# Kernel optimization log

Hardware: AMD Instinct MI355X
Metric: run time of the kernel (lower is better)

Reference implementation:

```python
import jax, jax.numpy as jnp
import numpy as np

BEV_H = 100
BEV_W = 100
BEV_Z = 4
NUM_CAMS = 6
EMBED = 256
HF, WF = 32, 88
PC_RANGE = (-51.2, -51.2, -5.0, 51.2, 51.2, 3.0)
EPS = 1e-5


def setup_inputs() -> dict:
    key = jax.random.key(0)
    ks = jax.random.split(key, 5)
    B, Nq = 1, BEV_H * BEV_W
    return {
        "query": jax.random.normal(ks[0], (B, Nq, EMBED), jnp.float32),
        "img_feats": jax.random.normal(ks[1], (B, NUM_CAMS, EMBED, HF, WF), jnp.float32),
        "lidar2img": jax.random.normal(ks[2], (B, NUM_CAMS, 4, 4), jnp.float32),
        "attn_w": jax.random.normal(ks[3], (EMBED, NUM_CAMS * BEV_Z), jnp.float32) * 0.02,
        "attn_b": jnp.zeros((NUM_CAMS * BEV_Z,), jnp.float32),
        "out_w": jax.random.normal(ks[4], (EMBED, EMBED), jnp.float32) * 0.02,
        "out_b": jnp.zeros((EMBED,), jnp.float32),
    }


def _reference_points(B):
    # normalized pillar reference points: (B, Nq, Z, 3), x,y,z in (0,1)
    ys = jnp.linspace(0.5, BEV_H - 0.5, BEV_H, dtype=jnp.float32) / BEV_H
    xs = jnp.linspace(0.5, BEV_W - 0.5, BEV_W, dtype=jnp.float32) / BEV_W
    ref_y, ref_x = jnp.meshgrid(ys, xs, indexing="ij")  # (H, W)
    Nq = BEV_H * BEV_W
    rx = jnp.broadcast_to(ref_x.reshape(Nq, 1), (Nq, BEV_Z))
    ry = jnp.broadcast_to(ref_y.reshape(Nq, 1), (Nq, BEV_Z))
    rz = jnp.broadcast_to(
        (jnp.linspace(0.5, BEV_Z - 0.5, BEV_Z, dtype=jnp.float32) / BEV_Z)[None, :],
        (Nq, BEV_Z),
    )
    ref = jnp.stack([rx, ry, rz], axis=-1)  # (Nq, Z, 3)
    return jnp.broadcast_to(ref[None], (B, Nq, BEV_Z, 3))


def _grid_sample(img, grid):
    # Bilinear grid_sample, zero padding, align_corners=False.
    # img: (M, C, H, W), grid: (M, N, 2) in [-1, 1] -> (M, C, N)
    M, C, H, W = img.shape
    x = ((grid[..., 0] + 1.0) * W - 1.0) * 0.5
    y = ((grid[..., 1] + 1.0) * H - 1.0) * 0.5
    x0 = jnp.floor(x)
    y0 = jnp.floor(y)
    wx1 = x - x0
    wy1 = y - y0

    def tap(xi, yi, w):
        valid = (xi >= 0) & (xi < W) & (yi >= 0) & (yi < H)
        xc = jnp.clip(xi, 0, W - 1).astype(jnp.int32)
        yc = jnp.clip(yi, 0, H - 1).astype(jnp.int32)
        v = jax.vmap(lambda im, yy, xx: im[:, yy, xx])(img, yc, xc)  # (M, C, N)
        return v * (w * valid)[:, None, :]

    return (
        tap(x0, y0, (1.0 - wx1) * (1.0 - wy1))
        + tap(x0 + 1.0, y0, wx1 * (1.0 - wy1))
        + tap(x0, y0 + 1.0, (1.0 - wx1) * wy1)
        + tap(x0 + 1.0, y0 + 1.0, wx1 * wy1)
    )


def reference(query, img_feats, lidar2img, attn_w, attn_b, out_w, out_b):
    B, Nq, C = query.shape
    Ncam = img_feats.shape[1]
    Hf, Wf = img_feats.shape[-2], img_feats.shape[-1]
    Z = BEV_Z

    ref = _reference_points(B)  # (B, Nq, Z, 3)
    pc = PC_RANGE
    scale = jnp.array([pc[3] - pc[0], pc[4] - pc[1], pc[5] - pc[2]], jnp.float32)
    offset = jnp.array([pc[0], pc[1], pc[2]], jnp.float32)
    r = ref * scale + offset
    r4 = jnp.concatenate([r, jnp.ones_like(r[..., :1])], axis=-1).reshape(B, Nq * Z, 4)

    # project to each camera: (B, Ncam, Nq*Z, 4)
    cam = jnp.einsum("bnij,bqj->bnqi", lidar2img, r4)
    depth = cam[..., 2]
    xy = cam[..., 0:2] / jnp.maximum(depth, EPS)[..., None]
    gx = (xy[..., 0] / (Wf - 1) - 0.5) * 2.0
    gy = (xy[..., 1] / (Hf - 1) - 0.5) * 2.0
    grid = jnp.stack([gx, gy], axis=-1)  # (B, Ncam, Nq*Z, 2)
    valid = (depth > EPS) & (gx > -1.0) & (gx < 1.0) & (gy > -1.0) & (gy < 1.0)

    sampled = _grid_sample(
        img_feats.reshape(B * Ncam, C, Hf, Wf), grid.reshape(B * Ncam, Nq * Z, 2)
    )  # (B*Ncam, C, Nq*Z)
    sampled = sampled.reshape(B, Ncam, C, Nq, Z) * valid.reshape(B, Ncam, 1, Nq, Z)
    sampled = jnp.nan_to_num(sampled)

    # (cam, z) softmax weights from the query
    w = jax.nn.softmax(query @ attn_w + attn_b, axis=-1).reshape(B, Nq, Ncam, Z)
    out = jnp.einsum("bncqz,bqnz->bqc", sampled, w)
    out = out @ out_w + out_b
    return out + query
```

## Files before the change

### kernel.cpp

```cpp
#include <hip/hip_runtime.h>
#include <math.h>

#define NCAM 6
#define CH   256
#define HFt  32
#define WFt  88
#define NQ   10000
#define NPT  24

typedef __attribute__((ext_vector_type(8))) short short8;
typedef __attribute__((ext_vector_type(4))) float f32x4;

__device__ __forceinline__ unsigned short f2bf(float x) {
  unsigned int u = __float_as_uint(x);
  u += 0x7FFFu + ((u >> 16) & 1u);
  return (unsigned short)(u >> 16);
}
__device__ __forceinline__ float bf2f(unsigned short b) {
  return __uint_as_float(((unsigned int)b) << 16);
}

#define TRBLKS  (NCAM * HFt * 4)
#define WSWBLKS 32
#define LOGITS0 (TRBLKS + WSWBLKS)
#define NLB     157

__global__ __launch_bounds__(256) void k_prep(const float* __restrict__ img,
                                              const float* __restrict__ query,
                                              const float* __restrict__ aw,
                                              const float* __restrict__ ab,
                                              const float* __restrict__ ow,
                                              unsigned short* __restrict__ featT,
                                              unsigned short* __restrict__ Wsw,
                                              float* __restrict__ Wgt) {
  __shared__ __align__(16) char smem[50176];
  const int blk = blockIdx.x;
  const int tid = threadIdx.x;

  if (blk < TRBLKS) {
    float (*tile)[89] = (float(*)[89])smem;
    int ct = blk & 3, h = (blk >> 2) & 31, cam = blk >> 7;
    const float* src = img + (((size_t)cam * CH + ct * 64) * HFt + h) * WFt;
    for (int i = tid; i < 64 * WFt; i += 256) {
      int c = i / WFt, w = i - c * WFt;
      tile[c][w] = src[(size_t)c * (HFt * WFt) + w];
    }
    __syncthreads();
    unsigned short* dst = featT + ((size_t)(cam * HFt + h) * WFt) * CH + ct * 64;
    for (int i = tid; i < WFt * 32; i += 256) {
      int w = i >> 5, cp = i & 31;
      unsigned int u = (unsigned int)f2bf(tile[2 * cp][w]) |
                       ((unsigned int)f2bf(tile[2 * cp + 1][w]) << 16);
      *(unsigned int*)(dst + (size_t)w * CH + 2 * cp) = u;
    }
    return;
  }

  if (blk < LOGITS0) {
    int gtid = (blk - TRBLKS) * 256 + tid;
    int l  = gtid & 63;
    int f  = (gtid >> 6) & 1;
    int kk = (gtid >> 7) & 7;
    int c  = gtid >> 10;
    int n  = 32 * c + 16 * f + (l & 15);
    int kb = 32 * kk + 4 * (l >> 4);
    unsigned int u0 = f2bf(ow[(kb + 0) * CH + n])  | ((unsigned int)f2bf(ow[(kb + 1) * CH + n])  << 16);
    unsigned int u1 = f2bf(ow[(kb + 2) * CH + n])  | ((unsigned int)f2bf(ow[(kb + 3) * CH + n])  << 16);
    unsigned int u2 = f2bf(ow[(kb + 16) * CH + n]) | ((unsigned int)f2bf(ow[(kb + 17) * CH + n]) << 16);
    unsigned int u3 = f2bf(ow[(kb + 18) * CH + n]) | ((unsigned int)f2bf(ow[(kb + 19) * CH + n]) << 16);
    ((uint4*)Wsw)[gtid] = make_uint4(u0, u1, u2, u3);
    return;
  }

  const int q0 = (blk - LOGITS0) * 64;
  uint4*          awB = (uint4*)smem;
  unsigned short* As  = (unsigned short*)(smem + 16384);

  for (int i = tid; i < 64 * 64; i += 256) {
    int row = i >> 6, g = i & 63;
    int qq = q0 + row;
    float4 v = (qq < NQ) ? *(const float4*)(query + (size_t)qq * CH + 4 * g)
                         : make_float4(0.f, 0.f, 0.f, 0.f);
    ushort4 s4;
    s4.x = f2bf(v.x); s4.y = f2bf(v.y); s4.z = f2bf(v.z); s4.w = f2bf(v.w);
    *(ushort4*)(As + row * 264 + 4 * g) = s4;
  }
  for (int e = tid; e < 1024; e += 256) {
    int l = e & 63, f = (e >> 6) & 1, kk = e >> 7;
    int n = 16 * f + (l & 15);
    int kb = 32 * kk + 4 * (l >> 4);
    uint4 u = make_uint4(0u, 0u, 0u, 0u);
    if (n < NPT) {
      u.x = f2bf(aw[(kb + 0) * NPT + n])  | ((unsigned int)f2bf(aw[(kb + 1) * NPT + n])  << 16);
      u.y = f2bf(aw[(kb + 2) * NPT + n])  | ((unsigned int)f2bf(aw[(kb + 3) * NPT + n])  << 16);
      u.z = f2bf(aw[(kb + 16) * NPT + n]) | ((unsigned int)f2bf(aw[(kb + 17) * NPT + n]) << 16);
      u.w = f2bf(aw[(kb + 18) * NPT + n]) | ((unsigned int)f2bf(aw[(kb + 19) * NPT + n]) << 16);
    }
    awB[e] = u;
  }
  __syncthreads();

  const int wv = tid >> 6, l = tid & 63;
  const int col = l & 15, grp = l >> 4;

  short8 af[8];
  const unsigned short* ap = As + (wv * 16 + col) * 264 + 4 * grp;
#pragma unroll
  for (int kk = 0; kk < 8; kk++) {
    uint2 lo = *(const uint2*)(ap + kk * 32);
    uint2 hi = *(const uint2*)(ap + kk * 32 + 16);
    union { uint4 u; short8 s; } x;
    x.u.x = lo.x; x.u.y = lo.y; x.u.z = hi.x; x.u.w = hi.y;
    af[kk] = x.s;
  }
  f32x4 acc0 = {0.f, 0.f, 0.f, 0.f}, acc1 = {0.f, 0.f, 0.f, 0.f};
#pragma unroll
  for (int kk = 0; kk < 8; kk++) {
    union { uint4 u; short8 s; } b0, b1;
    b0.u = awB[(kk * 2 + 0) * 64 + l];
    b1.u = awB[(kk * 2 + 1) * 64 + l];
    acc0 = __builtin_amdgcn_mfma_f32_16x16x32_bf16(af[kk], b0.s, acc0, 0, 0, 0);
    acc1 = __builtin_amdgcn_mfma_f32_16x16x32_bf16(af[kk], b1.s, acc1, 0, 0, 0);
  }

  const int n0 = col, n1 = 16 + col;
  const bool v16 = (n1 < NPT);
  const float ab0 = ab[n0];
  const float ab1 = v16 ? ab[n1] : 0.f;
#pragma unroll
  for (int r = 0; r < 4; r++) {
    float v0 = acc0[r] + ab0;
    float v1 = v16 ? (acc1[r] + ab1) : -3.4e38f;
    float m = fmaxf(v0, v1);
#pragma unroll
    for (int off = 1; off < 16; off <<= 1) m = fmaxf(m, __shfl_xor(m, off, 64));
    float e0 = __expf(v0 - m);
    float e1 = v16 ? __expf(v1 - m) : 0.f;
    float s = e0 + e1;
#pragma unroll
    for (int off = 1; off < 16; off <<= 1) s += __shfl_xor(s, off, 64);
    int qq = q0 + wv * 16 + 4 * grp + r;
    if (qq < NQ) {
      Wgt[qq * NPT + n0] = e0 / s;
      if (v16) Wgt[qq * NPT + n1] = e1 / s;
    }
  }
}

__global__ __launch_bounds__(256) void k_main(const unsigned short* __restrict__ featT,
                                              const float* __restrict__ l2i,
                                              const float* __restrict__ Wgt,
                                              unsigned short* __restrict__ A) {
  const int wv   = threadIdx.x >> 6;
  const int lane = threadIdx.x & 63;
  const int q    = blockIdx.x * 4 + wv;

  __shared__ float Lm[NCAM * 16];
  __shared__ int   offW[4][96];
  __shared__ float wW[4][96];

  if (threadIdx.x < NCAM * 16) Lm[threadIdx.x] = l2i[threadIdx.x];

  float sw = (lane < NPT) ? Wgt[q * NPT + lane] : 0.f;

  __syncthreads();

  bool valid = false;
  int o0 = 0, o1 = 0, o2 = 0, o3 = 0;
  float w0 = 0.f, w1 = 0.f, w2 = 0.f, w3 = 0.f;
  if (lane < NPT) {
    int cam = lane >> 2, z = lane & 3;
    float X  = (((q % 100) + 0.5f) * 0.01f) * 102.4f - 51.2f;
    float Y  = (((q / 100) + 0.5f) * 0.01f) * 102.4f - 51.2f;
    float Zc = ((z + 0.5f) * 0.25f) * 8.f - 5.f;
    const float* Lr = Lm + cam * 16;
    float cx = Lr[0] * X + Lr[1] * Y + Lr[2]  * Zc + Lr[3];
    float cy = Lr[4] * X + Lr[5] * Y + Lr[6]  * Zc + Lr[7];
    float cd = Lr[8] * X + Lr[9] * Y + Lr[10] * Zc + Lr[11];
    float d  = fmaxf(cd, 1e-5f);
    float gx = (cx / d * (1.f / 87.f) - 0.5f) * 2.f;
    float gy = (cy / d * (1.f / 31.f) - 0.5f) * 2.f;
    valid = (cd > 1e-5f) && (gx > -1.f) && (gx < 1.f) && (gy > -1.f) && (gy < 1.f);

    float x = ((gx + 1.f) * 88.f - 1.f) * 0.5f;
    float y = ((gy + 1.f) * 32.f - 1.f) * 0.5f;
    float x0f = floorf(x), y0f = floorf(y);
    float wx1 = x - x0f, wy1 = y - y0f;
    float wx0 = 1.f - wx1, wy0 = 1.f - wy1;
    bool vx0 = (x0f >= 0.f) && (x0f < 88.f);
    bool vx1 = (x0f + 1.f >= 0.f) && (x0f + 1.f < 88.f);
    bool vy0 = (y0f >= 0.f) && (y0f < 32.f);
    bool vy1 = (y0f + 1.f >= 0.f) && (y0f + 1.f < 32.f);
    int x0 = (int)fminf(fmaxf(x0f, 0.f), 87.f);
    int x1 = (int)fminf(fmaxf(x0f + 1.f, 0.f), 87.f);
    int y0 = (int)fminf(fmaxf(y0f, 0.f), 31.f);
    int y1 = (int)fminf(fmaxf(y0f + 1.f, 0.f), 31.f);
    int cb = cam * (HFt * WFt);
    o0 = (cb + y0 * WFt + x0) * CH;
    o1 = (cb + y0 * WFt + x1) * CH;
    o2 = (cb + y1 * WFt + x0) * CH;
    o3 = (cb + y1 * WFt + x1) * CH;
    w0 = sw * wx0 * wy0 * ((vx0 && vy0) ? 1.f : 0.f);
    w1 = sw * wx1 * wy0 * ((vx1 && vy0) ? 1.f : 0.f);
    w2 = sw * wx0 * wy1 * ((vx0 && vy1) ? 1.f : 0.f);
    w3 = sw * wx1 * wy1 * ((vx1 && vy1) ? 1.f : 0.f);
  }

  unsigned long long vm = __ballot(valid);
  int nvalid = __popcll(vm);
  int pos = __popcll(vm & ((1ull << lane) - 1ull));
  if (valid) {
    int b = 4 * pos;
    offW[wv][b + 0] = o0; wW[wv][b + 0] = w0;
    offW[wv][b + 1] = o1; wW[wv][b + 1] = w1;
    offW[wv][b + 2] = o2; wW[wv][b + 2] = w2;
    offW[wv][b + 3] = o3; wW[wv][b + 3] = w3;
  }
  int nt  = 4 * nvalid;
  int ntp = (nt + 7) & ~7;
  if (lane < ntp - nt) { offW[wv][nt + lane] = 0; wW[wv][nt + lane] = 0.f; }

  float4 acc0 = {0.f, 0.f, 0.f, 0.f}, acc1 = {0.f, 0.f, 0.f, 0.f};
  const unsigned short* fb = featT + 4 * lane;
  for (int i = 0; i < ntp; i += 8) {
    int   a0 = offW[wv][i + 0], a1 = offW[wv][i + 1], a2 = offW[wv][i + 2], a3 = offW[wv][i + 3];
    int   a4 = offW[wv][i + 4], a5 = offW[wv][i + 5], a6 = offW[wv][i + 6], a7 = offW[wv][i + 7];
    float b0 = wW[wv][i + 0], b1 = wW[wv][i + 1], b2 = wW[wv][i + 2], b3 = wW[wv][i + 3];
    float b4 = wW[wv][i + 4], b5 = wW[wv][i + 5], b6 = wW[wv][i + 6], b7 = wW[wv][i + 7];
    ushort4 v0 = *(const ushort4*)(fb + a0);
    ushort4 v1 = *(const ushort4*)(fb + a1);
    ushort4 v2 = *(const ushort4*)(fb + a2);
    ushort4 v3 = *(const ushort4*)(fb + a3);
    ushort4 v4 = *(const ushort4*)(fb + a4);
    ushort4 v5 = *(const ushort4*)(fb + a5);
    ushort4 v6 = *(const ushort4*)(fb + a6);
    ushort4 v7 = *(const ushort4*)(fb + a7);
    acc0.x = fmaf(b0, bf2f(v0.x), acc0.x); acc0.y = fmaf(b0, bf2f(v0.y), acc0.y);
    acc0.z = fmaf(b0, bf2f(v0.z), acc0.z); acc0.w = fmaf(b0, bf2f(v0.w), acc0.w);
    acc1.x = fmaf(b1, bf2f(v1.x), acc1.x); acc1.y = fmaf(b1, bf2f(v1.y), acc1.y);
    acc1.z = fmaf(b1, bf2f(v1.z), acc1.z); acc1.w = fmaf(b1, bf2f(v1.w), acc1.w);
    acc0.x = fmaf(b2, bf2f(v2.x), acc0.x); acc0.y = fmaf(b2, bf2f(v2.y), acc0.y);
    acc0.z = fmaf(b2, bf2f(v2.z), acc0.z); acc0.w = fmaf(b2, bf2f(v2.w), acc0.w);
    acc1.x = fmaf(b3, bf2f(v3.x), acc1.x); acc1.y = fmaf(b3, bf2f(v3.y), acc1.y);
    acc1.z = fmaf(b3, bf2f(v3.z), acc1.z); acc1.w = fmaf(b3, bf2f(v3.w), acc1.w);
    acc0.x = fmaf(b4, bf2f(v4.x), acc0.x); acc0.y = fmaf(b4, bf2f(v4.y), acc0.y);
    acc0.z = fmaf(b4, bf2f(v4.z), acc0.z); acc0.w = fmaf(b4, bf2f(v4.w), acc0.w);
    acc1.x = fmaf(b5, bf2f(v5.x), acc1.x); acc1.y = fmaf(b5, bf2f(v5.y), acc1.y);
    acc1.z = fmaf(b5, bf2f(v5.z), acc1.z); acc1.w = fmaf(b5, bf2f(v5.w), acc1.w);
    acc0.x = fmaf(b6, bf2f(v6.x), acc0.x); acc0.y = fmaf(b6, bf2f(v6.y), acc0.y);
    acc0.z = fmaf(b6, bf2f(v6.z), acc0.z); acc0.w = fmaf(b6, bf2f(v6.w), acc0.w);
    acc1.x = fmaf(b7, bf2f(v7.x), acc1.x); acc1.y = fmaf(b7, bf2f(v7.y), acc1.y);
    acc1.z = fmaf(b7, bf2f(v7.z), acc1.z); acc1.w = fmaf(b7, bf2f(v7.w), acc1.w);
  }
  ushort4 st;
  st.x = f2bf(acc0.x + acc1.x); st.y = f2bf(acc0.y + acc1.y);
  st.z = f2bf(acc0.z + acc1.z); st.w = f2bf(acc0.w + acc1.w);
  *(ushort4*)(A + (size_t)q * CH + 4 * lane) = st;
}

#define ASP 264
__global__ __launch_bounds__(256) void k_out_mfma(const unsigned short* __restrict__ A,
                                                  const float* __restrict__ query,
                                                  const unsigned short* __restrict__ Wsw,
                                                  const float* __restrict__ ob,
                                                  float* __restrict__ outp) {
  const int blk = blockIdx.x;
  const int mtile = blk >> 1, nhalf = blk & 1;
  const int m0 = mtile * 16;
  const int t = threadIdx.x, wv = t >> 6, l = t & 63;
  const int row = l & 15, grp = l >> 4;

  __shared__ unsigned short As[16 * ASP];

  {
    const uint4* src = (const uint4*)(A + (size_t)m0 * CH);
    uint4 v0 = src[t];
    uint4 v1 = src[t + 256];
    int r0 = t >> 5, c0 = t & 31;
    int g1 = t + 256; int r1 = g1 >> 5, c1 = g1 & 31;
    *(uint4*)(&As[r0 * ASP + c0 * 8]) = v0;
    *(uint4*)(&As[r1 * ASP + c1 * 8]) = v1;
  }
  __syncthreads();

  short8 af[8];
  {
    const unsigned short* ap = &As[row * ASP + 4 * grp];
#pragma unroll
    for (int kk = 0; kk < 8; kk++) {
      uint2 lo = *(const uint2*)(ap + kk * 32);
      uint2 hi = *(const uint2*)(ap + kk * 32 + 16);
      union { uint4 u; short8 s; } x;
      x.u.x = lo.x; x.u.y = lo.y; x.u.z = hi.x; x.u.w = hi.y;
      af[kk] = x.s;
    }
  }

  const int chunk = nhalf * 4 + wv;
  const uint4* wp = (const uint4*)Wsw;
  f32x4 acc0 = {0.f, 0.f, 0.f, 0.f}, acc1 = {0.f, 0.f, 0.f, 0.f};
#pragma unroll
  for (int kk = 0; kk < 8; kk++) {
    uint4 w0 = wp[((chunk * 8 + kk) * 2 + 0) * 64 + l];
    uint4 w1 = wp[((chunk * 8 + kk) * 2 + 1) * 64 + l];
    union { uint4 u; short8 s; } b0, b1;
    b0.u = w0; b1.u = w1;
    acc0 = __builtin_amdgcn_mfma_f32_16x16x32_bf16(af[kk], b0.s, acc0, 0, 0, 0);
    acc1 = __builtin_amdgcn_mfma_f32_16x16x32_bf16(af[kk], b1.s, acc1, 0, 0, 0);
  }

  const int nbase = nhalf * 128 + wv * 32;
#pragma unroll
  for (int f = 0; f < 2; f++) {
    f32x4 ac = (f == 0) ? acc0 : acc1;
    int n = nbase + 16 * f + row;
    float bias = ob[n];
#pragma unroll
    for (int r = 0; r < 4; r++) {
      int m = m0 + 4 * grp + r;
      size_t idx = (size_t)m * CH + n;
      outp[idx] = ac[r] + bias + query[idx];
    }
  }
}

extern "C" void kernel_launch(void* const* d_in, const int* in_sizes, int n_in,
                              void* d_out, int out_size, void* d_ws, size_t ws_size,
                              hipStream_t stream) {
  const float* query = (const float*)d_in[0];
  const float* img   = (const float*)d_in[1];
  const float* l2i   = (const float*)d_in[2];
  const float* aw    = (const float*)d_in[3];
  const float* ab    = (const float*)d_in[4];
  const float* ow    = (const float*)d_in[5];
  const float* ob    = (const float*)d_in[6];
  float* outp = (float*)d_out;

  char* ws = (char*)d_ws;
  unsigned short* featT = (unsigned short*)ws;
  unsigned short* Abf   = (unsigned short*)(ws + 8650752);
  unsigned short* Wsw   = (unsigned short*)(ws + 13770752);
  float*          Wgt   = (float*)(ws + 13901824);

  k_prep<<<TRBLKS + WSWBLKS + NLB, 256, 0, stream>>>(img, query, aw, ab, ow, featT, Wsw, Wgt);
  k_main<<<NQ / 4, 256, 0, stream>>>(featT, l2i, Wgt, Abf);
  k_out_mfma<<<(NQ / 16) * 2, 256, 0, stream>>>(Abf, query, Wsw, ob, outp);
}
```

Baseline: 35.49 us.

## Fuse bilinear sampling kernel with output projection MFMA kernel

Merges the per-query sampling kernel and the bf16 MFMA output projection into one kernel. Each 256-thread block now handles 16 queries: every wave gathers 4 queries into a shared-memory tile, then each wave computes 64 output columns with MFMA. This removes the global round trip of the intermediate bf16 activation buffer and one kernel launch. In exchange there are fewer blocks (625 instead of 2500), and each wave runs its four queries' gathers in sequence, which may lower latency hiding.

Measured after the change: 36.99 us. 1.04x slower.

```diff
diff --git a/kernel.cpp b/kernel.cpp
--- a/kernel.cpp
+++ b/kernel.cpp
@@ -147,145 +147,140 @@
   }
 }
 
-__global__ __launch_bounds__(256) void k_main(const unsigned short* __restrict__ featT,
-                                              const float* __restrict__ l2i,
-                                              const float* __restrict__ Wgt,
-                                              unsigned short* __restrict__ A) {
-  const int wv   = threadIdx.x >> 6;
-  const int lane = threadIdx.x & 63;
-  const int q    = blockIdx.x * 4 + wv;
+#define QPB 16
+__global__ __launch_bounds__(256) void k_fused(const unsigned short* __restrict__ featT,
+                                               const float* __restrict__ l2i,
+                                               const float* __restrict__ Wgt,
+                                               const float* __restrict__ query,
+                                               const unsigned short* __restrict__ Wsw,
+                                               const float* __restrict__ ob,
+                                               float* __restrict__ outp) {
+  const int blk = blockIdx.x;
+  const int q0 = blk * QPB;
+  const int t = threadIdx.x, wv = t >> 6, l = t & 63;
 
   __shared__ float Lm[NCAM * 16];
-  __shared__ int   offW[4][96];
-  __shared__ float wW[4][96];
-
-  if (threadIdx.x < NCAM * 16) Lm[threadIdx.x] = l2i[threadIdx.x];
-
-  float sw = (lane < NPT) ? Wgt[q * NPT + lane] : 0.f;
+  __shared__ int   offW[QPB][96];
+  __shared__ float wW[QPB][96];
+  __shared__ __align__(16) unsigned short Atile[QPB * 264];
+
+  if (t < NCAM * 16) Lm[t] = l2i[t];
+
+  float swA[4];
+#pragma unroll
+  for (int p = 0; p < 4; p++)
+    swA[p] = (l < NPT) ? Wgt[(q0 + 4 * wv + p) * NPT + l] : 0.f;
 
   __syncthreads();
 
-  bool valid = false;
-  int o0 = 0, o1 = 0, o2 = 0, o3 = 0;
-  float w0 = 0.f, w1 = 0.f, w2 = 0.f, w3 = 0.f;
-  if (lane < NPT) {
-    int cam = lane >> 2, z = lane & 3;
-    float X  = (((q % 100) + 0.5f) * 0.01f) * 102.4f - 51.2f;
-    float Y  = (((q / 100) + 0.5f) * 0.01f) * 102.4f - 51.2f;
-    float Zc = ((z + 0.5f) * 0.25f) * 8.f - 5.f;
-    const float* Lr = Lm + cam * 16;
-    float cx = Lr[0] * X + Lr[1] * Y + Lr[2]  * Zc + Lr[3];
-    float cy = Lr[4] * X + Lr[5] * Y + Lr[6]  * Zc + Lr[7];
-    float cd = Lr[8] * X + Lr[9] * Y + Lr[10] * Zc + Lr[11];
-    float d  = fmaxf(cd, 1e-5f);
-    float gx = (cx / d * (1.f / 87.f) - 0.5f) * 2.f;
-    float gy = (cy / d * (1.f / 31.f) - 0.5f) * 2.f;
-    valid = (cd > 1e-5f) && (gx > -1.f) && (gx < 1.f) && (gy > -1.f) && (gy < 1.f);
-
-    float x = ((gx + 1.f) * 88.f - 1.f) * 0.5f;
-    float y = ((gy + 1.f) * 32.f - 1.f) * 0.5f;
-    float x0f = floorf(x), y0f = floorf(y);
-    float wx1 = x - x0f, wy1 = y - y0f;
-    float wx0 = 1.f - wx1, wy0 = 1.f - wy1;
-    bool vx0 = (x0f >= 0.f) && (x0f < 88.f);
-    bool vx1 = (x0f + 1.f >= 0.f) && (x0f + 1.f < 88.f);
-    bool vy0 = (y0f >= 0.f) && (y0f < 32.f);
-    bool vy1 = (y0f + 1.f >= 0.f) && (y0f + 1.f < 32.f);
-    int x0 = (int)fminf(fmaxf(x0f, 0.f), 87.f);
-    int x1 = (int)fminf(fmaxf(x0f + 1.f, 0.f), 87.f);
-    int y0 = (int)fminf(fmaxf(y0f, 0.f), 31.f);
-    int y1 = (int)fminf(fmaxf(y0f + 1.f, 0.f), 31.f);
-    int cb = cam * (HFt * WFt);
-    o0 = (cb + y0 * WFt + x0) * CH;
-    o1 = (cb + y0 * WFt + x1) * CH;
-    o2 = (cb + y1 * WFt + x0) * CH;
-    o3 = (cb + y1 * WFt + x1) * CH;
-    w0 = sw * wx0 * wy0 * ((vx0 && vy0) ? 1.f : 0.f);
-    w1 = sw * wx1 * wy0 * ((vx1 && vy0) ? 1.f : 0.f);
-    w2 = sw * wx0 * wy1 * ((vx0 && vy1) ? 1.f : 0.f);
-    w3 = sw * wx1 * wy1 * ((vx1 && vy1) ? 1.f : 0.f);
-  }
-
-  unsigned long long vm = __ballot(valid);
-  int nvalid = __popcll(vm);
-  int pos = __popcll(vm & ((1ull << lane) - 1ull));
-  if (valid) {
-    int b = 4 * pos;
-    offW[wv][b + 0] = o0; wW[wv][b + 0] = w0;
-    offW[wv][b + 1] = o1; wW[wv][b + 1] = w1;
-    offW[wv][b + 2] = o2; wW[wv][b + 2] = w2;
-    offW[wv][b + 3] = o3; wW[wv][b + 3] = w3;
-  }
-  int nt  = 4 * nvalid;
-  int ntp = (nt + 7) & ~7;
-  if (lane < ntp - nt) { offW[wv][nt + lane] = 0; wW[wv][nt + lane] = 0.f; }
-
-  float4 acc0 = {0.f, 0.f, 0.f, 0.f}, acc1 = {0.f, 0.f, 0.f, 0.f};
-  const unsigned short* fb = featT + 4 * lane;
-  for (int i = 0; i < ntp; i += 8) {
-    int   a0 = offW[wv][i + 0], a1 = offW[wv][i + 1], a2 = offW[wv][i + 2], a3 = offW[wv][i + 3];
-    int   a4 = offW[wv][i + 4], a5 = offW[wv][i + 5], a6 = offW[wv][i + 6], a7 = offW[wv][i + 7];
-    float b0 = wW[wv][i + 0], b1 = wW[wv][i + 1], b2 = wW[wv][i + 2], b3 = wW[wv][i + 3];
-    float b4 = wW[wv][i + 4], b5 = wW[wv][i + 5], b6 = wW[wv][i + 6], b7 = wW[wv][i + 7];
-    ushort4 v0 = *(const ushort4*)(fb + a0);
-    ushort4 v1 = *(const ushort4*)(fb + a1);
-    ushort4 v2 = *(const ushort4*)(fb + a2);
-    ushort4 v3 = *(const ushort4*)(fb + a3);
-    ushort4 v4 = *(const ushort4*)(fb + a4);
-    ushort4 v5 = *(const ushort4*)(fb + a5);
-    ushort4 v6 = *(const ushort4*)(fb + a6);
-    ushort4 v7 = *(const ushort4*)(fb + a7);
-    acc0.x = fmaf(b0, bf2f(v0.x), acc0.x); acc0.y = fmaf(b0, bf2f(v0.y), acc0.y);
-    acc0.z = fmaf(b0, bf2f(v0.z), acc0.z); acc0.w = fmaf(b0, bf2f(v0.w), acc0.w);
-    acc1.x = fmaf(b1, bf2f(v1.x), acc1.x); acc1.y = fmaf(b1, bf2f(v1.y), acc1.y);
-    acc1.z = fmaf(b1, bf2f(v1.z), acc1.z); acc1.w = fmaf(b1, bf2f(v1.w), acc1.w);
-    acc0.x = fmaf(b2, bf2f(v2.x), acc0.x); acc0.y = fmaf(b2, bf2f(v2.y), acc0.y);
-    acc0.z = fmaf(b2, bf2f(v2.z), acc0.z); acc0.w = fmaf(b2, bf2f(v2.w), acc0.w);
-    acc1.x = fmaf(b3, bf2f(v3.x), acc1.x); acc1.y = fmaf(b3, bf2f(v3.y), acc1.y);
-    acc1.z = fmaf(b3, bf2f(v3.z), acc1.z); acc1.w = fmaf(b3, bf2f(v3.w), acc1.w);
-    acc0.x = fmaf(b4, bf2f(v4.x), acc0.x); acc0.y = fmaf(b4, bf2f(v4.y), acc0.y);
-    acc0.z = fmaf(b4, bf2f(v4.z), acc0.z); acc0.w = fmaf(b4, bf2f(v4.w), acc0.w);
-    acc1.x = fmaf(b5, bf2f(v5.x), acc1.x); acc1.y = fmaf(b5, bf2f(v5.y), acc1.y);
-    acc1.z = fmaf(b5, bf2f(v5.z), acc1.z); acc1.w = fmaf(b5, bf2f(v5.w), acc1.w);
-    acc0.x = fmaf(b6, bf2f(v6.x), acc0.x); acc0.y = fmaf(b6, bf2f(v6.y), acc0.y);
-    acc0.z = fmaf(b6, bf2f(v6.z), acc0.z); acc0.w = fmaf(b6, bf2f(v6.w), acc0.w);
-    acc1.x = fmaf(b7, bf2f(v7.x), acc1.x); acc1.y = fmaf(b7, bf2f(v7.y), acc1.y);
-    acc1.z = fmaf(b7, bf2f(v7.z), acc1.z); acc1.w = fmaf(b7, bf2f(v7.w), acc1.w);
-  }
-  ushort4 st;
-  st.x = f2bf(acc0.x + acc1.x); st.y = f2bf(acc0.y + acc1.y);
-  st.z = f2bf(acc0.z + acc1.z); st.w = f2bf(acc0.w + acc1.w);
-  *(ushort4*)(A + (size_t)q * CH + 4 * lane) = st;
-}
-
-#define ASP 264
-__global__ __launch_bounds__(256) void k_out_mfma(const unsigned short* __restrict__ A,
-                                                  const float* __restrict__ query,
-                                                  const unsigned short* __restrict__ Wsw,
-                                                  const float* __restrict__ ob,
-                                                  float* __restrict__ outp) {
-  const int blk = blockIdx.x;
-  const int mtile = blk >> 1, nhalf = blk & 1;
-  const int m0 = mtile * 16;
-  const int t = threadIdx.x, wv = t >> 6, l = t & 63;
-  const int row = l & 15, grp = l >> 4;
-
-  __shared__ unsigned short As[16 * ASP];
-
-  {
-    const uint4* src = (const uint4*)(A + (size_t)m0 * CH);
-    uint4 v0 = src[t];
-    uint4 v1 = src[t + 256];
-    int r0 = t >> 5, c0 = t & 31;
-    int g1 = t + 256; int r1 = g1 >> 5, c1 = g1 & 31;
-    *(uint4*)(&As[r0 * ASP + c0 * 8]) = v0;
-    *(uint4*)(&As[r1 * ASP + c1 * 8]) = v1;
+  int ntpA[4];
+#pragma unroll
+  for (int p = 0; p < 4; p++) {
+    const int g = 4 * wv + p;
+    const int q = q0 + g;
+    bool valid = false;
+    int o0 = 0, o1 = 0, o2 = 0, o3 = 0;
+    float w0 = 0.f, w1 = 0.f, w2 = 0.f, w3 = 0.f;
+    if (l < NPT) {
+      int cam = l >> 2, z = l & 3;
+      float X  = (((q % 100) + 0.5f) * 0.01f) * 102.4f - 51.2f;
+      float Y  = (((q / 100) + 0.5f) * 0.01f) * 102.4f - 51.2f;
+      float Zc = ((z + 0.5f) * 0.25f) * 8.f - 5.f;
+      const float* Lr = Lm + cam * 16;
+      float cx = Lr[0] * X + Lr[1] * Y + Lr[2]  * Zc + Lr[3];
+      float cy = Lr[4] * X + Lr[5] * Y + Lr[6]  * Zc + Lr[7];
+      float cd = Lr[8] * X + Lr[9] * Y + Lr[10] * Zc + Lr[11];
+      float d  = fmaxf(cd, 1e-5f);
+      float gx = (cx / d * (1.f / 87.f) - 0.5f) * 2.f;
+      float gy = (cy / d * (1.f / 31.f) - 0.5f) * 2.f;
+      valid = (cd > 1e-5f) && (gx > -1.f) && (gx < 1.f) && (gy > -1.f) && (gy < 1.f);
+
+      float x = ((gx + 1.f) * 88.f - 1.f) * 0.5f;
+      float y = ((gy + 1.f) * 32.f - 1.f) * 0.5f;
+      float x0f = floorf(x), y0f = floorf(y);
+      float wx1 = x - x0f, wy1 = y - y0f;
+      float wx0 = 1.f - wx1, wy0 = 1.f - wy1;
+      bool vx0 = (x0f >= 0.f) && (x0f < 88.f);
+      bool vx1 = (x0f + 1.f >= 0.f) && (x0f + 1.f < 88.f);
+      bool vy0 = (y0f >= 0.f) && (y0f < 32.f);
+      bool vy1 = (y0f + 1.f >= 0.f) && (y0f + 1.f < 32.f);
+      int x0 = (int)fminf(fmaxf(x0f, 0.f), 87.f);
+      int x1 = (int)fminf(fmaxf(x0f + 1.f, 0.f), 87.f);
+      int y0 = (int)fminf(fmaxf(y0f, 0.f), 31.f);
+      int y1 = (int)fminf(fmaxf(y0f + 1.f, 0.f), 31.f);
+      int cb = cam * (HFt * WFt);
+      float sw = swA[p];
+      o0 = (cb + y0 * WFt + x0) * CH;
+      o1 = (cb + y0 * WFt + x1) * CH;
+      o2 = (cb + y1 * WFt + x0) * CH;
+      o3 = (cb + y1 * WFt + x1) * CH;
+      w0 = sw * wx0 * wy0 * ((vx0 && vy0) ? 1.f : 0.f);
+      w1 = sw * wx1 * wy0 * ((vx1 && vy0) ? 1.f : 0.f);
+      w2 = sw * wx0 * wy1 * ((vx0 && vy1) ? 1.f : 0.f);
+      w3 = sw * wx1 * wy1 * ((vx1 && vy1) ? 1.f : 0.f);
+    }
+    unsigned long long vm = __ballot(valid);
+    int nvalid = __popcll(vm);
+    int pos = __popcll(vm & ((1ull << l) - 1ull));
+    if (valid) {
+      int b = 4 * pos;
+      offW[g][b + 0] = o0; wW[g][b + 0] = w0;
+      offW[g][b + 1] = o1; wW[g][b + 1] = w1;
+      offW[g][b + 2] = o2; wW[g][b + 2] = w2;
+      offW[g][b + 3] = o3; wW[g][b + 3] = w3;
+    }
+    int nt  = 4 * nvalid;
+    int ntp = (nt + 7) & ~7;
+    if (l < ntp - nt) { offW[g][nt + l] = 0; wW[g][nt + l] = 0.f; }
+    ntpA[p] = ntp;
+  }
+
+  const unsigned short* fb = featT + 4 * l;
+#pragma unroll
+  for (int p = 0; p < 4; p++) {
+    const int g = 4 * wv + p;
+    float4 acc0 = {0.f, 0.f, 0.f, 0.f}, acc1 = {0.f, 0.f, 0.f, 0.f};
+    for (int i = 0; i < ntpA[p]; i += 8) {
+      int   a0 = offW[g][i + 0], a1 = offW[g][i + 1], a2 = offW[g][i + 2], a3 = offW[g][i + 3];
+      int   a4 = offW[g][i + 4], a5 = offW[g][i + 5], a6 = offW[g][i + 6], a7 = offW[g][i + 7];
+      float b0 = wW[g][i + 0], b1 = wW[g][i + 1], b2 = wW[g][i + 2], b3 = wW[g][i + 3];
+      float b4 = wW[g][i + 4], b5 = wW[g][i + 5], b6 = wW[g][i + 6], b7 = wW[g][i + 7];
+      ushort4 v0 = *(const ushort4*)(fb + a0);
+      ushort4 v1 = *(const ushort4*)(fb + a1);
+      ushort4 v2 = *(const ushort4*)(fb + a2);
+      ushort4 v3 = *(const ushort4*)(fb + a3);
+      ushort4 v4 = *(const ushort4*)(fb + a4);
+      ushort4 v5 = *(const ushort4*)(fb + a5);
+      ushort4 v6 = *(const ushort4*)(fb + a6);
+      ushort4 v7 = *(const ushort4*)(fb + a7);
+      acc0.x = fmaf(b0, bf2f(v0.x), acc0.x); acc0.y = fmaf(b0, bf2f(v0.y), acc0.y);
+      acc0.z = fmaf(b0, bf2f(v0.z), acc0.z); acc0.w = fmaf(b0, bf2f(v0.w), acc0.w);
+      acc1.x = fmaf(b1, bf2f(v1.x), acc1.x); acc1.y = fmaf(b1, bf2f(v1.y), acc1.y);
+      acc1.z = fmaf(b1, bf2f(v1.z), acc1.z); acc1.w = fmaf(b1, bf2f(v1.w), acc1.w);
+      acc0.x = fmaf(b2, bf2f(v2.x), acc0.x); acc0.y = fmaf(b2, bf2f(v2.y), acc0.y);
+      acc0.z = fmaf(b2, bf2f(v2.z), acc0.z); acc0.w = fmaf(b2, bf2f(v2.w), acc0.w);
+      acc1.x = fmaf(b3, bf2f(v3.x), acc1.x); acc1.y = fmaf(b3, bf2f(v3.y), acc1.y);
+      acc1.z = fmaf(b3, bf2f(v3.z), acc1.z); acc1.w = fmaf(b3, bf2f(v3.w), acc1.w);
+      acc0.x = fmaf(b4, bf2f(v4.x), acc0.x); acc0.y = fmaf(b4, bf2f(v4.y), acc0.y);
+      acc0.z = fmaf(b4, bf2f(v4.z), acc0.z); acc0.w = fmaf(b4, bf2f(v4.w), acc0.w);
+      acc1.x = fmaf(b5, bf2f(v5.x), acc1.x); acc1.y = fmaf(b5, bf2f(v5.y), acc1.y);
+      acc1.z = fmaf(b5, bf2f(v5.z), acc1.z); acc1.w = fmaf(b5, bf2f(v5.w), acc1.w);
+      acc0.x = fmaf(b6, bf2f(v6.x), acc0.x); acc0.y = fmaf(b6, bf2f(v6.y), acc0.y);
+      acc0.z = fmaf(b6, bf2f(v6.z), acc0.z); acc0.w = fmaf(b6, bf2f(v6.w), acc0.w);
+      acc1.x = fmaf(b7, bf2f(v7.x), acc1.x); acc1.y = fmaf(b7, bf2f(v7.y), acc1.y);
+      acc1.z = fmaf(b7, bf2f(v7.z), acc1.z); acc1.w = fmaf(b7, bf2f(v7.w), acc1.w);
+    }
+    ushort4 st;
+    st.x = f2bf(acc0.x + acc1.x); st.y = f2bf(acc0.y + acc1.y);
+    st.z = f2bf(acc0.z + acc1.z); st.w = f2bf(acc0.w + acc1.w);
+    *(ushort4*)(Atile + g * 264 + 4 * l) = st;
   }
   __syncthreads();
 
+  const int col = l & 15, grp = l >> 4;
   short8 af[8];
   {
-    const unsigned short* ap = &As[row * ASP + 4 * grp];
+    const unsigned short* ap = Atile + col * 264 + 4 * grp;
 #pragma unroll
     for (int kk = 0; kk < 8; kk++) {
       uint2 lo = *(const uint2*)(ap + kk * 32);
@@ -295,29 +290,31 @@
       af[kk] = x.s;
     }
   }
-
-  const int chunk = nhalf * 4 + wv;
   const uint4* wp = (const uint4*)Wsw;
-  f32x4 acc0 = {0.f, 0.f, 0.f, 0.f}, acc1 = {0.f, 0.f, 0.f, 0.f};
+  f32x4 oa0 = {0.f,0.f,0.f,0.f}, oa1 = {0.f,0.f,0.f,0.f};
+  f32x4 oa2 = {0.f,0.f,0.f,0.f}, oa3 = {0.f,0.f,0.f,0.f};
 #pragma unroll
   for (int kk = 0; kk < 8; kk++) {
-    uint4 w0 = wp[((chunk * 8 + kk) * 2 + 0) * 64 + l];
-    uint4 w1 = wp[((chunk * 8 + kk) * 2 + 1) * 64 + l];
-    union { uint4 u; short8 s; } b0, b1;
-    b0.u = w0; b1.u = w1;
-    acc0 = __builtin_amdgcn_mfma_f32_16x16x32_bf16(af[kk], b0.s, acc0, 0, 0, 0);
-    acc1 = __builtin_amdgcn_mfma_f32_16x16x32_bf16(af[kk], b1.s, acc1, 0, 0, 0);
-  }
-
-  const int nbase = nhalf * 128 + wv * 32;
-#pragma unroll
-  for (int f = 0; f < 2; f++) {
-    f32x4 ac = (f == 0) ? acc0 : acc1;
-    int n = nbase + 16 * f + row;
+    const int c0 = 2 * wv, c1 = 2 * wv + 1;
+    union { uint4 u; short8 s; } b0, b1, b2, b3;
+    b0.u = wp[((c0 * 8 + kk) * 2 + 0) * 64 + l];
+    b1.u = wp[((c0 * 8 + kk) * 2 + 1) * 64 + l];
+    b2.u = wp[((c1 * 8 + kk) * 2 + 0) * 64 + l];
+    b3.u = wp[((c1 * 8 + kk) * 2 + 1) * 64 + l];
+    oa0 = __builtin_amdgcn_mfma_f32_16x16x32_bf16(af[kk], b0.s, oa0, 0, 0, 0);
+    oa1 = __builtin_amdgcn_mfma_f32_16x16x32_bf16(af[kk], b1.s, oa1, 0, 0, 0);
+    oa2 = __builtin_amdgcn_mfma_f32_16x16x32_bf16(af[kk], b2.s, oa2, 0, 0, 0);
+    oa3 = __builtin_amdgcn_mfma_f32_16x16x32_bf16(af[kk], b3.s, oa3, 0, 0, 0);
+  }
+
+#pragma unroll
+  for (int f = 0; f < 4; f++) {
+    f32x4 ac = (f == 0) ? oa0 : (f == 1) ? oa1 : (f == 2) ? oa2 : oa3;
+    int n = 64 * wv + 16 * f + col;
     float bias = ob[n];
 #pragma unroll
     for (int r = 0; r < 4; r++) {
-      int m = m0 + 4 * grp + r;
+      int m = q0 + 4 * grp + r;
       size_t idx = (size_t)m * CH + n;
       outp[idx] = ac[r] + bias + query[idx];
     }
@@ -338,11 +335,9 @@
 
   char* ws = (char*)d_ws;
   unsigned short* featT = (unsigned short*)ws;
-  unsigned short* Abf   = (unsigned short*)(ws + 8650752);
-  unsigned short* Wsw   = (unsigned short*)(ws + 13770752);
-  float*          Wgt   = (float*)(ws + 13901824);
+  unsigned short* Wsw   = (unsigned short*)(ws + 8650752);
+  float*          Wgt   = (float*)(ws + 8781824);
 
   k_prep<<<TRBLKS + WSWBLKS + NLB, 256, 0, stream>>>(img, query, aw, ab, ow, featT, Wsw, Wgt);
-  k_main<<<NQ / 4, 256, 0, stream>>>(featT, l2i, Wgt, Abf);
-  k_out_mfma<<<(NQ / 16) * 2, 256, 0, stream>>>(Abf, query, Wsw, ob, outp);
-}
+  k_fused<<<NQ / QPB, 256, 0, stream>>>(featT, l2i, Wgt, query, Wsw, ob, outp);
+}
```

## Shrink prep shared memory, vectorize transpose loads, read query fragments directly

Applied to the files above, without the earlier changes.

The transpose part of the prep kernel now uses 32-channel tiles (twice as many blocks), float4 global loads and 8-byte bf16 stores. The logits part drops the shared-memory staging of the query tile and loads each lane's MFMA A fragment straight from global memory, converting to bf16 in registers. Together these cut static LDS from about 49KB to 16KB so more blocks can be resident per CU. The trade-off is more blocks to launch and less coalesced global reads of the query.

Result: faster. 30.98 us, median of 2 (-12.7%).

```diff
diff --git a/kernel.cpp b/kernel.cpp
--- a/kernel.cpp
+++ b/kernel.cpp
@@ -20,7 +20,7 @@
   return __uint_as_float(((unsigned int)b) << 16);
 }
 
-#define TRBLKS  (NCAM * HFt * 4)
+#define TRBLKS  (NCAM * HFt * 8)
 #define WSWBLKS 32
 #define LOGITS0 (TRBLKS + WSWBLKS)
 #define NLB     157
@@ -33,25 +33,30 @@
                                               unsigned short* __restrict__ featT,
                                               unsigned short* __restrict__ Wsw,
                                               float* __restrict__ Wgt) {
-  __shared__ __align__(16) char smem[50176];
+  __shared__ __align__(16) char smem[16384];
   const int blk = blockIdx.x;
   const int tid = threadIdx.x;
 
   if (blk < TRBLKS) {
-    float (*tile)[89] = (float(*)[89])smem;
-    int ct = blk & 3, h = (blk >> 2) & 31, cam = blk >> 7;
-    const float* src = img + (((size_t)cam * CH + ct * 64) * HFt + h) * WFt;
-    for (int i = tid; i < 64 * WFt; i += 256) {
-      int c = i / WFt, w = i - c * WFt;
-      tile[c][w] = src[(size_t)c * (HFt * WFt) + w];
+    float (*tile)[WFt + 1] = (float (*)[WFt + 1])smem;
+    int ct = blk & 7, h = (blk >> 3) & 31, cam = blk >> 8;
+    const float* src = img + (((size_t)cam * CH + ct * 32) * HFt + h) * WFt;
+    for (int i = tid; i < 32 * 22; i += 256) {
+      int c = i / 22, w4 = i - c * 22;
+      float4 v = *(const float4*)(src + (size_t)c * (HFt * WFt) + 4 * w4);
+      tile[c][4 * w4 + 0] = v.x;
+      tile[c][4 * w4 + 1] = v.y;
+      tile[c][4 * w4 + 2] = v.z;
+      tile[c][4 * w4 + 3] = v.w;
     }
     __syncthreads();
-    unsigned short* dst = featT + ((size_t)(cam * HFt + h) * WFt) * CH + ct * 64;
-    for (int i = tid; i < WFt * 32; i += 256) {
-      int w = i >> 5, cp = i & 31;
-      unsigned int u = (unsigned int)f2bf(tile[2 * cp][w]) |
-                       ((unsigned int)f2bf(tile[2 * cp + 1][w]) << 16);
-      *(unsigned int*)(dst + (size_t)w * CH + 2 * cp) = u;
+    unsigned short* dst = featT + ((size_t)(cam * HFt + h) * WFt) * CH + ct * 32;
+    for (int i = tid; i < WFt * 8; i += 256) {
+      int w = i >> 3, g = i & 7;
+      uint2 u;
+      u.x = (unsigned int)f2bf(tile[4 * g + 0][w]) | ((unsigned int)f2bf(tile[4 * g + 1][w]) << 16);
+      u.y = (unsigned int)f2bf(tile[4 * g + 2][w]) | ((unsigned int)f2bf(tile[4 * g + 3][w]) << 16);
+      *(uint2*)(dst + (size_t)w * CH + 4 * g) = u;
     }
     return;
   }
@@ -73,54 +78,43 @@
   }
 
   const int q0 = (blk - LOGITS0) * 64;
-  uint4*          awB = (uint4*)smem;
-  unsigned short* As  = (unsigned short*)(smem + 16384);
-
-  for (int i = tid; i < 64 * 64; i += 256) {
-    int row = i >> 6, g = i & 63;
-    int qq = q0 + row;
-    float4 v = (qq < NQ) ? *(const float4*)(query + (size_t)qq * CH + 4 * g)
-                         : make_float4(0.f, 0.f, 0.f, 0.f);
-    ushort4 s4;
-    s4.x = f2bf(v.x); s4.y = f2bf(v.y); s4.z = f2bf(v.z); s4.w = f2bf(v.w);
-    *(ushort4*)(As + row * 264 + 4 * g) = s4;
-  }
+  uint4* awB = (uint4*)smem;
   for (int e = tid; e < 1024; e += 256) {
-    int l = e & 63, f = (e >> 6) & 1, kk = e >> 7;
-    int n = 16 * f + (l & 15);
-    int kb = 32 * kk + 4 * (l >> 4);
-    uint4 u = make_uint4(0u, 0u, 0u, 0u);
+    int le = e & 63, f = (e >> 6) & 1, kk = e >> 7;
+    int n = 16 * f + (le & 15);
+    int kb = 32 * kk + 4 * (le >> 4);
+    uint4 uv = make_uint4(0u, 0u, 0u, 0u);
     if (n < NPT) {
-      u.x = f2bf(aw[(kb + 0) * NPT + n])  | ((unsigned int)f2bf(aw[(kb + 1) * NPT + n])  << 16);
-      u.y = f2bf(aw[(kb + 2) * NPT + n])  | ((unsigned int)f2bf(aw[(kb + 3) * NPT + n])  << 16);
-      u.z = f2bf(aw[(kb + 16) * NPT + n]) | ((unsigned int)f2bf(aw[(kb + 17) * NPT + n]) << 16);
-      u.w = f2bf(aw[(kb + 18) * NPT + n]) | ((unsigned int)f2bf(aw[(kb + 19) * NPT + n]) << 16);
-    }
-    awB[e] = u;
+      uv.x = f2bf(aw[(kb + 0) * NPT + n])  | ((unsigned int)f2bf(aw[(kb + 1) * NPT + n])  << 16);
+      uv.y = f2bf(aw[(kb + 2) * NPT + n])  | ((unsigned int)f2bf(aw[(kb + 3) * NPT + n])  << 16);
+      uv.z = f2bf(aw[(kb + 16) * NPT + n]) | ((unsigned int)f2bf(aw[(kb + 17) * NPT + n]) << 16);
+      uv.w = f2bf(aw[(kb + 18) * NPT + n]) | ((unsigned int)f2bf(aw[(kb + 19) * NPT + n]) << 16);
+    }
+    awB[e] = uv;
   }
   __syncthreads();
 
   const int wv = tid >> 6, l = tid & 63;
   const int col = l & 15, grp = l >> 4;
-
-  short8 af[8];
-  const unsigned short* ap = As + (wv * 16 + col) * 264 + 4 * grp;
+  int qr = q0 + wv * 16 + col;
+  if (qr > NQ - 1) qr = NQ - 1;
+  const float* qp = query + (size_t)qr * CH + 4 * grp;
+
+  f32x4 acc0 = {0.f, 0.f, 0.f, 0.f}, acc1 = {0.f, 0.f, 0.f, 0.f};
 #pragma unroll
   for (int kk = 0; kk < 8; kk++) {
-    uint2 lo = *(const uint2*)(ap + kk * 32);
-    uint2 hi = *(const uint2*)(ap + kk * 32 + 16);
-    union { uint4 u; short8 s; } x;
-    x.u.x = lo.x; x.u.y = lo.y; x.u.z = hi.x; x.u.w = hi.y;
-    af[kk] = x.s;
-  }
-  f32x4 acc0 = {0.f, 0.f, 0.f, 0.f}, acc1 = {0.f, 0.f, 0.f, 0.f};
-#pragma unroll
-  for (int kk = 0; kk < 8; kk++) {
+    float4 lo = *(const float4*)(qp + kk * 32);
+    float4 hi = *(const float4*)(qp + kk * 32 + 16);
+    union { uint4 u; short8 s; } a;
+    a.u.x = (unsigned int)f2bf(lo.x) | ((unsigned int)f2bf(lo.y) << 16);
+    a.u.y = (unsigned int)f2bf(lo.z) | ((unsigned int)f2bf(lo.w) << 16);
+    a.u.z = (unsigned int)f2bf(hi.x) | ((unsigned int)f2bf(hi.y) << 16);
+    a.u.w = (unsigned int)f2bf(hi.z) | ((unsigned int)f2bf(hi.w) << 16);
     union { uint4 u; short8 s; } b0, b1;
     b0.u = awB[(kk * 2 + 0) * 64 + l];
     b1.u = awB[(kk * 2 + 1) * 64 + l];
-    acc0 = __builtin_amdgcn_mfma_f32_16x16x32_bf16(af[kk], b0.s, acc0, 0, 0, 0);
-    acc1 = __builtin_amdgcn_mfma_f32_16x16x32_bf16(af[kk], b1.s, acc1, 0, 0, 0);
+    acc0 = __builtin_amdgcn_mfma_f32_16x16x32_bf16(a.s, b0.s, acc0, 0, 0, 0);
+    acc1 = __builtin_amdgcn_mfma_f32_16x16x32_bf16(a.s, b1.s, acc1, 0, 0, 0);
   }
 
   const int n0 = col, n1 = 16 + col;
```
